# Performance work log

Hardware: AMD Instinct MI355X
Metric: run time of the kernel (lower is better)

The kernel has to match this reference:

```python
import jax, jax.numpy as jnp
import numpy as np
from math import sqrt

NUM_CLASSES = 21
TOP_K = 200
CONF_THRESH = 0.01
NMS_THRESH = 0.45
VAR0, VAR1 = 0.1, 0.2
FMAPS = [19, 10, 5, 3, 2, 1]
INPUT_SIZE = 300
STEPS = [16, 32, 64, 100, 150, 300]
MIN_SIZES = [60, 105, 150, 195, 240, 285]
MAX_SIZES = [105, 150, 195, 240, 285, 330]
ASPECT_RATIOS = [[2, 3]] * 6


def _create_priorbox():
    # Faithful numpy port of create_priorbox (runs once at setup).
    mean = []
    for k, f in enumerate(FMAPS):
        f_k = INPUT_SIZE / STEPS[k]
        s_k = MIN_SIZES[k] / INPUT_SIZE
        s_kp = sqrt(s_k * (MAX_SIZES[k] / INPUT_SIZE))
        for i in range(f):
            for j in range(f):
                cx = (j + 0.5) / f_k
                cy = (i + 0.5) / f_k
                mean.append([cx, cy, s_k, s_k])
                mean.append([cx, cy, s_kp, s_kp])
                for ar in ASPECT_RATIOS[k]:
                    r = sqrt(ar)
                    mean.append([cx, cy, s_k * r, s_k / r])
                    mean.append([cx, cy, s_k / r, s_k * r])
    return np.clip(np.asarray(mean, dtype=np.float32), 0.0, 1.0)  # [3000, 4]


def setup_inputs() -> dict:
    key = jax.random.key(0)
    k1, k2 = jax.random.split(key)
    B, P, C = 8, 3000, NUM_CLASSES
    loc_data = jax.random.normal(k1, (B, P, 4), jnp.float32)
    conf_data = jax.random.uniform(k2, (B, P, C), jnp.float32)  # post-softmax-like probs
    priors = jnp.asarray(_create_priorbox())
    return {"loc_data": loc_data, "conf_data": conf_data, "priors": priors}


def _decode(loc, priors):
    # SSD box decode: center-offset form -> corner form. loc, priors: [P, 4]
    cxcy = priors[:, :2] + loc[:, :2] * VAR0 * priors[:, 2:]
    wh = priors[:, 2:] * jnp.exp(loc[:, 2:] * VAR1)
    xy1 = cxcy - 0.5 * wh
    return jnp.concatenate([xy1, xy1 + wh], axis=-1)  # [P, 4] (x1, y1, x2, y2)


def _iou_matrix(b):
    # b: [P, 4] corner-form boxes -> [P, P] pairwise IoU
    area = (b[:, 2] - b[:, 0]) * (b[:, 3] - b[:, 1])
    lt = jnp.maximum(b[:, None, :2], b[None, :, :2])
    rb = jnp.minimum(b[:, None, 2:], b[None, :, 2:])
    wh = jnp.clip(rb - lt, 0.0)
    inter = wh[..., 0] * wh[..., 1]
    union = area[:, None] + area[None, :] - inter
    return inter / jnp.maximum(union, 1e-12)


def _nms_one_class(scores, boxes):
    # scores: [P], boxes: [P, 4]. Greedy hard NMS over threshold-passing boxes,
    # kept detections (in score order) padded to TOP_K rows of [score, x1, y1, x2, y2].
    P = scores.shape[0]
    valid = scores > CONF_THRESH
    s = jnp.where(valid, scores, -jnp.inf)
    order = jnp.argsort(-s)  # descending by score; invalid sorted last
    ss = s[order]
    sb = boxes[order]
    sv = valid[order]
    iou = _iou_matrix(sb)  # [P, P]
    idx = jnp.arange(P)

    def body(i, keep):
        sup = keep[i] & (iou[i] > NMS_THRESH) & (idx > i)
        return keep & ~sup

    keep = jax.lax.stop_gradient(jax.lax.fori_loop(0, P, body, sv))
    # first TOP_K kept candidates, preserving score order
    sel = jnp.argsort(jnp.where(keep, idx, idx + P))[:TOP_K]
    ok = keep[sel]
    out_s = jnp.where(ok, ss[sel], 0.0)
    out_b = jnp.where(ok[:, None], sb[sel], 0.0)
    return jnp.concatenate([out_s[:, None], out_b], axis=-1)  # [TOP_K, 5]


def _per_image(loc, conf, priors):
    boxes = _decode(loc, priors)  # [P, 4]
    cls_scores = conf.T[1:]  # skip background class 0 -> [C-1, P]
    dets = jax.vmap(lambda s: _nms_one_class(s, boxes))(cls_scores)  # [C-1, TOP_K, 5]
    bg = jnp.zeros((1, TOP_K, 5), dets.dtype)
    return jnp.concatenate([bg, dets], axis=0)  # [C, TOP_K, 5]


def reference(loc_data, conf_data, priors):
    # lax.map over batch keeps peak memory to one image's IoU matrices.
    # NOTE: the original's final flt[(rank < top_k)].fill_(0) is a no-op in
    # PyTorch (advanced indexing returns a copy), so output is returned as-is.
    out = jax.lax.map(lambda lc: _per_image(lc[0], lc[1], priors), (loc_data, conf_data))
    return out  # [B, NUM_CLASSES, TOP_K, 5]
```

## Files before the change

### kernel.cpp

```cpp
#include <hip/hip_runtime.h>
#include <math.h>

#pragma clang fp contract(off)

#define PNUM    3000
#define NCLS    21
#define TOPK    200
#define BLOCK   1024
#define CHUNK   1024
#define NMS_T   0.45f
#define LO_BITS 0x3C23D70Bu
#define HI_BITS 0x3F800001u
#define MAXKEEP (TOPK + 64)

__device__ __constant__ unsigned LADDER[15] = {
    0x3F333333u, 0x3F266666u, 0x3F19999Au, 0x3F0CCCCDu, 0x3F000000u,
    0x3EE66666u, 0x3ECCCCCDu, 0x3EB33333u, 0x3E99999Au, 0x3E800000u,
    0x3E4CCCCDu, 0x3E19999Au, 0x3DCCCCCDu, 0x3D4CCCCDu, LO_BITS };

__device__ __forceinline__ float iou_f(float4 a, float aa, float4 b, float ab) {
    float ltx = fmaxf(a.x, b.x);
    float lty = fmaxf(a.y, b.y);
    float rbx = fminf(a.z, b.z);
    float rby = fminf(a.w, b.w);
    float iw  = fmaxf(rbx - ltx, 0.0f);
    float ih  = fmaxf(rby - lty, 0.0f);
    float inter = iw * ih;
    float uni   = aa + ab - inter;
    return inter / fmaxf(uni, 1e-12f);
}

__global__ __launch_bounds__(BLOCK) void ssd_nms_kernel(
    const float* __restrict__ loc,
    const float* __restrict__ conf,
    const float* __restrict__ priors,
    float* __restrict__ out)
{
    const int c   = blockIdx.x;
    const int b   = blockIdx.y;
    const int tid = threadIdx.x;

    float* outbase = out + ((size_t)(b * NCLS + c)) * (TOPK * 5);

    if (c == 0) {
        for (int i = tid; i < TOPK * 5; i += BLOCK) outbase[i] = 0.0f;
        return;
    }

    __shared__ unsigned long long s_bufA[CHUNK];
    __shared__ unsigned long long s_bufB[CHUNK];
    __shared__ float4             s_box[CHUNK];
    __shared__ float              s_area[CHUNK];
    __shared__ float              s_score[CHUNK];
    __shared__ float4             s_kb[MAXKEEP];
    __shared__ float              s_ka[MAXKEEP];
    __shared__ unsigned long long s_supT[2][16][64];
    __shared__ unsigned long long s_deadT[2][16];
    __shared__ int                s_wcnt[16];
    __shared__ int s_m;

    const int lane = tid & 63;
    const int wav  = tid >> 6;

    unsigned hb[4];
    const float* confb = conf + ((size_t)b * PNUM) * NCLS + c;
    #pragma unroll
    for (int q = 0; q < 4; ++q) {
        int i = tid + (q << 10);
        unsigned h = 0u;
        if (i < PNUM) {
            float s = confb[(size_t)i * NCLS];
            if (s > 0.01f) h = __float_as_uint(s);
        }
        hb[q] = h;
    }

    unsigned Thi = HI_BITS;
    int rung = 0;
    int cnt = 0;
    bool done = false;

    for (;;) {
        unsigned T = LADDER[rung];

        __syncthreads();
        if (tid == 0) s_m = 0;
        s_bufA[tid] = 0ull;
        __syncthreads();
        #pragma unroll
        for (int q = 0; q < 4; ++q) {
            unsigned sb = hb[q];
            bool p = (sb >= T && sb < Thi);
            unsigned long long bal = __ballot(p);
            int wb = 0;
            if (lane == 0 && bal) wb = atomicAdd(&s_m, (int)__popcll(bal));
            wb = __shfl(wb, 0);
            if (p) {
                int dst = wb + (int)__popcll(bal & ((1ull << lane) - 1ull));
                if (dst < CHUNK) {
                    int i = tid + (q << 10);
                    s_bufA[dst] = ((unsigned long long)sb << 32) | (unsigned)(~i);
                }
            }
        }
        __syncthreads();
        int M = s_m;

        if (M > CHUNK) {
            unsigned lo = T + 1, hi = Thi;
            while (lo < hi) {
                unsigned mid = lo + ((hi - lo) >> 1);
                __syncthreads();
                int c2 = 0;
                #pragma unroll
                for (int q = 0; q < 4; ++q)
                    c2 += (int)__popcll(__ballot(hb[q] >= mid && hb[q] < Thi));
                if (lane == 0) s_wcnt[wav] = c2;
                __syncthreads();
                int n = 0;
                #pragma unroll
                for (int w = 0; w < 16; ++w) n += s_wcnt[w];
                if (n <= CHUNK) hi = mid; else lo = mid + 1;
            }
            T = hi;
            __syncthreads();
            int wc = 0;
            #pragma unroll
            for (int q = 0; q < 4; ++q)
                wc += (int)__popcll(__ballot(hb[q] >= T && hb[q] < Thi));
            if (lane == 0) s_wcnt[wav] = wc;
            s_bufA[tid] = 0ull;
            __syncthreads();
            int wbase = 0; M = 0;
            #pragma unroll
            for (int w = 0; w < 16; ++w) {
                int v = s_wcnt[w];
                M += v;
                if (w < wav) wbase += v;
            }
            int base = wbase;
            #pragma unroll
            for (int q = 0; q < 4; ++q) {
                unsigned sb = hb[q];
                bool p = (sb >= T && sb < Thi);
                unsigned long long bal = __ballot(p);
                if (p) {
                    int dst = base + (int)__popcll(bal & ((1ull << lane) - 1ull));
                    int i = tid + (q << 10);
                    s_bufA[dst] = ((unsigned long long)sb << 32) | (unsigned)(~i);
                }
                base += (int)__popcll(bal);
            }
            __syncthreads();
        }

        if (M == 0) {
            if (T <= LO_BITS) break;
            Thi = T;
            while (rung < 14 && LADDER[rung] >= T) rung++;
            continue;
        }

        unsigned N = 64;
        while (N < (unsigned)M) N <<= 1;
        unsigned long long key = s_bufA[tid];
        int parity = 0;
        for (unsigned k = 2; k <= N; k <<= 1) {
            for (unsigned j = k >> 1; j > 0; j >>= 1) {
                unsigned long long pk;
                if (j >= 64) {
                    unsigned long long* buf = parity ? s_bufB : s_bufA;
                    buf[tid] = key;
                    __syncthreads();
                    pk = buf[tid ^ j];
                    parity ^= 1;
                } else {
                    pk = __shfl_xor(key, (int)j, 64);
                }
                bool takeMax  = (((tid & j) == 0) == ((tid & k) == 0));
                bool pGreater = pk > key;
                if (takeMax == pGreater) key = pk;
            }
        }

        if (key != 0ull) {
            unsigned idx = ~(unsigned)key;
            float4 l  = ((const float4*)loc)[(size_t)b * PNUM + idx];
            float4 pr = ((const float4*)priors)[idx];
            float cx = pr.x + l.x * 0.1f * pr.z;
            float cy = pr.y + l.y * 0.1f * pr.w;
            float w  = pr.z * expf(l.z * 0.2f);
            float h  = pr.w * expf(l.w * 0.2f);
            float x1 = cx - 0.5f * w;
            float y1 = cy - 0.5f * h;
            float x2 = x1 + w;
            float y2 = y1 + h;
            s_box[tid]   = make_float4(x1, y1, x2, y2);
            s_area[tid]  = (x2 - x1) * (y2 - y1);
            s_score[tid] = __uint_as_float((unsigned)(key >> 32));
        }
        __syncthreads();

        int pos = 0;
        int parityR = 0;
        while (pos < M) {
            int bn = M - pos; if (bn > 64) bn = 64;

            {
                unsigned long long bits = 0ull;
                bool bad = false;
                if (lane < bn) {
                    float4 bL = s_box[pos + lane];
                    float  aL = s_area[pos + lane];
                    #pragma unroll 2
                    for (int K = wav; K < cnt; K += 16)
                        bad |= (iou_f(s_kb[K], s_ka[K], bL, aL) > NMS_T);
                    int M0 = wav << 2;
                    #pragma unroll
                    for (int q2 = 0; q2 < 4; ++q2) {
                        int Mi = M0 + q2;
                        if (Mi < lane) {
                            if (iou_f(s_box[pos + Mi], s_area[pos + Mi], bL, aL) > NMS_T)
                                bits |= (1ull << Mi);
                        }
                    }
                }
                s_supT[parityR][wav][lane] = bits;
                unsigned long long db = __ballot(bad);
                if (lane == 0) s_deadT[parityR][wav] = db;
            }
            __syncthreads();

            unsigned long long own = 0ull, dead = 0ull;
            #pragma unroll
            for (int w = 0; w < 16; ++w) {
                own  |= s_supT[parityR][w][lane];
                dead |= s_deadT[parityR][w];
            }
            unsigned long long aliveM =
                ((bn == 64) ? ~0ull : ((1ull << bn) - 1ull)) & ~dead;
            bool alive = (aliveM >> lane) & 1ull;
            unsigned long long kept  = __ballot(alive && own == 0ull);
            unsigned long long undec = aliveM & ~kept;
            while (undec) {
                bool inU = (undec >> lane) & 1ull;
                bool dd  = inU && (own & kept) != 0ull;
                bool kk  = inU && (own & kept) == 0ull && (own & undec) == 0ull;
                unsigned long long nd = __ballot(dd);
                unsigned long long nk = __ballot(kk);
                kept  |= nk;
                undec &= ~(nd | nk);
            }

            int keptN = (int)__popcll(kept);
            if ((kept >> lane) & 1ull) {
                int krank = (int)__popcll(kept & ((1ull << lane) - 1ull));
                int kid = cnt + krank;
                int sl  = pos + lane;
                float4 bx = s_box[sl];
                s_kb[kid] = bx;
                s_ka[kid] = s_area[sl];
                if (wav == 0 && kid < TOPK) {
                    float* o = outbase + (size_t)kid * 5;
                    o[0] = s_score[sl];
                    o[1] = bx.x; o[2] = bx.y; o[3] = bx.z; o[4] = bx.w;
                }
            }
            cnt += keptN;
            if (cnt >= TOPK) { done = true; break; }
            pos += bn;
            parityR ^= 1;
        }

        if (done) break;
        if (T <= LO_BITS) break;
        Thi = T;
        while (rung < 14 && LADDER[rung] >= T) rung++;
    }

    __syncthreads();
    const int cf = cnt < TOPK ? cnt : TOPK;
    for (int r = cf + tid; r < TOPK; r += BLOCK) {
        float* o = outbase + (size_t)r * 5;
        o[0] = 0.f; o[1] = 0.f; o[2] = 0.f; o[3] = 0.f; o[4] = 0.f;
    }
}

extern "C" void kernel_launch(void* const* d_in, const int* in_sizes, int n_in,
                              void* d_out, int out_size, void* d_ws, size_t ws_size,
                              hipStream_t stream) {
    const float* loc    = (const float*)d_in[0];
    const float* conf   = (const float*)d_in[1];
    const float* priors = (const float*)d_in[2];
    float* out          = (float*)d_out;
    const int B = in_sizes[0] / (PNUM * 4);
    dim3 grid(NCLS, B);
    ssd_nms_kernel<<<grid, BLOCK, 0, stream>>>(loc, conf, priors, out);
}
```

Before: 93.13 us.

## Widen NMS batch to 128 candidates with two-word suppression masks

Each inner NMS step now resolves 128 sorted candidates instead of 64. The intra-batch IoU matrix is built row-wise with ballots into two 64-bit words per row, and the kept-box check is split so pairs of waves cover the two halves. The goal is to halve the number of block-wide barriers and batch rounds needed to reach the top-k kept boxes. In exchange the step does more speculative IoU work past the top-k cutoff and runs a more complex two-half fixpoint loop.

```diff
diff --git a/kernel.cpp b/kernel.cpp
--- a/kernel.cpp
+++ b/kernel.cpp
@@ -8,10 +8,11 @@
 #define TOPK    200
 #define BLOCK   1024
 #define CHUNK   1024
+#define BATCH   128
 #define NMS_T   0.45f
 #define LO_BITS 0x3C23D70Bu
 #define HI_BITS 0x3F800001u
-#define MAXKEEP (TOPK + 64)
+#define MAXKEEP (TOPK + BATCH)
 
 __device__ __constant__ unsigned LADDER[15] = {
     0x3F333333u, 0x3F266666u, 0x3F19999Au, 0x3F0CCCCDu, 0x3F000000u,
@@ -54,7 +55,7 @@
     __shared__ float              s_score[CHUNK];
     __shared__ float4             s_kb[MAXKEEP];
     __shared__ float              s_ka[MAXKEEP];
-    __shared__ unsigned long long s_supT[2][16][64];
+    __shared__ unsigned long long s_supT[2][BATCH][2];
     __shared__ unsigned long long s_deadT[2][16];
     __shared__ int                s_wcnt[16];
     __shared__ int s_m;
@@ -204,57 +205,86 @@
         int pos = 0;
         int parityR = 0;
         while (pos < M) {
-            int bn = M - pos; if (bn > 64) bn = 64;
+            int bn = M - pos; if (bn > BATCH) bn = BATCH;
 
             {
-                unsigned long long bits = 0ull;
+                int cid = ((wav & 1) << 6) | lane;
                 bool bad = false;
-                if (lane < bn) {
-                    float4 bL = s_box[pos + lane];
-                    float  aL = s_area[pos + lane];
+                if (cid < bn) {
+                    float4 bC = s_box[pos + cid];
+                    float  aC = s_area[pos + cid];
                     #pragma unroll 2
-                    for (int K = wav; K < cnt; K += 16)
-                        bad |= (iou_f(s_kb[K], s_ka[K], bL, aL) > NMS_T);
-                    int M0 = wav << 2;
-                    #pragma unroll
-                    for (int q2 = 0; q2 < 4; ++q2) {
-                        int Mi = M0 + q2;
-                        if (Mi < lane) {
-                            if (iou_f(s_box[pos + Mi], s_area[pos + Mi], bL, aL) > NMS_T)
-                                bits |= (1ull << Mi);
-                        }
-                    }
-                }
-                s_supT[parityR][wav][lane] = bits;
+                    for (int K = (wav >> 1); K < cnt; K += 8)
+                        bad |= (iou_f(s_kb[K], s_ka[K], bC, aC) > NMS_T);
+                }
                 unsigned long long db = __ballot(bad);
                 if (lane == 0) s_deadT[parityR][wav] = db;
             }
+            {
+                int i0 = pos + lane;        if (i0 >= M) i0 = pos;
+                int i1 = pos + 64 + lane;   if (i1 >= M) i1 = pos;
+                float4 bC0 = s_box[i0]; float aC0 = s_area[i0];
+                float4 bC1 = s_box[i1]; float aC1 = s_area[i1];
+                #pragma unroll
+                for (int rr = 0; rr < 8; ++rr) {
+                    int row = (wav << 3) | rr;
+                    if (row >= bn) break;
+                    float4 bR = s_box[pos + row];
+                    float  aR = s_area[pos + row];
+                    bool p0 = (lane < row) &&
+                              (iou_f(bC0, aC0, bR, aR) > NMS_T);
+                    bool p1 = (64 + lane < row) &&
+                              (iou_f(bC1, aC1, bR, aR) > NMS_T);
+                    unsigned long long b0 = __ballot(p0);
+                    unsigned long long b1 = __ballot(p1);
+                    if (lane == 0) {
+                        s_supT[parityR][row][0] = b0;
+                        s_supT[parityR][row][1] = b1;
+                    }
+                }
+            }
             __syncthreads();
 
-            unsigned long long own = 0ull, dead = 0ull;
+            unsigned long long dead0 = 0ull, dead1 = 0ull;
             #pragma unroll
-            for (int w = 0; w < 16; ++w) {
-                own  |= s_supT[parityR][w][lane];
-                dead |= s_deadT[parityR][w];
-            }
-            unsigned long long aliveM =
-                ((bn == 64) ? ~0ull : ((1ull << bn) - 1ull)) & ~dead;
-            bool alive = (aliveM >> lane) & 1ull;
-            unsigned long long kept  = __ballot(alive && own == 0ull);
-            unsigned long long undec = aliveM & ~kept;
-            while (undec) {
-                bool inU = (undec >> lane) & 1ull;
-                bool dd  = inU && (own & kept) != 0ull;
-                bool kk  = inU && (own & kept) == 0ull && (own & undec) == 0ull;
-                unsigned long long nd = __ballot(dd);
-                unsigned long long nk = __ballot(kk);
-                kept  |= nk;
-                undec &= ~(nd | nk);
-            }
-
-            int keptN = (int)__popcll(kept);
-            if ((kept >> lane) & 1ull) {
-                int krank = (int)__popcll(kept & ((1ull << lane) - 1ull));
+            for (int w = 0; w < 16; w += 2) {
+                dead0 |= s_deadT[parityR][w];
+                dead1 |= s_deadT[parityR][w + 1];
+            }
+            unsigned long long own0 = s_supT[parityR][lane][0];
+            unsigned long long o1lo = s_supT[parityR][64 + lane][0];
+            unsigned long long o1hi = s_supT[parityR][64 + lane][1];
+
+            int bn0 = bn < 64 ? bn : 64;
+            int bn1 = bn > 64 ? bn - 64 : 0;
+            unsigned long long am0 =
+                ((bn0 == 64) ? ~0ull : ((1ull << bn0) - 1ull)) & ~dead0;
+            unsigned long long am1 =
+                ((bn1 == 64) ? ~0ull : ((1ull << bn1) - 1ull)) & ~dead1;
+            bool alive0 = (am0 >> lane) & 1ull;
+            bool alive1 = (am1 >> lane) & 1ull;
+            unsigned long long kept0 = __ballot(alive0 && own0 == 0ull);
+            unsigned long long kept1 = __ballot(alive1 && o1lo == 0ull && o1hi == 0ull);
+            unsigned long long und0 = am0 & ~kept0;
+            unsigned long long und1 = am1 & ~kept1;
+            while (und0 | und1) {
+                bool iU0 = (und0 >> lane) & 1ull;
+                bool iU1 = (und1 >> lane) & 1ull;
+                bool d0 = iU0 && (own0 & kept0) != 0ull;
+                bool k0 = iU0 && (own0 & kept0) == 0ull && (own0 & und0) == 0ull;
+                unsigned long long hit1 = (o1lo & kept0) | (o1hi & kept1);
+                unsigned long long pen1 = (o1lo & und0)  | (o1hi & und1);
+                bool d1 = iU1 && hit1 != 0ull;
+                bool k1 = iU1 && hit1 == 0ull && pen1 == 0ull;
+                unsigned long long nk0 = __ballot(k0), nd0 = __ballot(d0);
+                unsigned long long nk1 = __ballot(k1), nd1 = __ballot(d1);
+                kept0 |= nk0; und0 &= ~(nk0 | nd0);
+                kept1 |= nk1; und1 &= ~(nk1 | nd1);
+            }
+
+            int n0 = (int)__popcll(kept0), n1 = (int)__popcll(kept1);
+            if ((kept0 >> lane) & 1ull) {
+                int krank = (int)__popcll(kept0 & ((1ull << lane) - 1ull));
                 int kid = cnt + krank;
                 int sl  = pos + lane;
                 float4 bx = s_box[sl];
@@ -266,7 +296,20 @@
                     o[1] = bx.x; o[2] = bx.y; o[3] = bx.z; o[4] = bx.w;
                 }
             }
-            cnt += keptN;
+            if ((kept1 >> lane) & 1ull) {
+                int krank = n0 + (int)__popcll(kept1 & ((1ull << lane) - 1ull));
+                int kid = cnt + krank;
+                int sl  = pos + 64 + lane;
+                float4 bx = s_box[sl];
+                s_kb[kid] = bx;
+                s_ka[kid] = s_area[sl];
+                if (wav == 1 && kid < TOPK) {
+                    float* o = outbase + (size_t)kid * 5;
+                    o[0] = s_score[sl];
+                    o[1] = bx.x; o[2] = bx.y; o[3] = bx.z; o[4] = bx.w;
+                }
+            }
+            cnt += n0 + n1;
             if (cnt >= TOPK) { done = true; break; }
             pos += bn;
             parityR ^= 1;
```

Result: no change. 94.34 us (+1.3%).
